# Kernel optimization log

Measured on AMD Instinct MI355X. Metric: run time of the kernel, lower is better.

The kernel has to match this reference:

```python
import jax, jax.numpy as jnp
import numpy as np

B, T, D, K = 64, 512, 1024, 50


def setup_inputs() -> dict:
    key = jax.random.key(0)
    ks = jax.random.split(key, 6)
    inputs = jax.random.normal(ks[0], (B, T, D), dtype=jnp.float32)
    mask = jnp.ones((B, T), dtype=jnp.int32)
    labels = jax.random.randint(ks[1], (B, T), 0, K)
    W = jax.random.normal(ks[2], (D, K), dtype=jnp.float32) / jnp.sqrt(jnp.float32(D))
    b = jnp.zeros((K,), dtype=jnp.float32)
    transitions = jax.random.normal(ks[3], (K, K), dtype=jnp.float32) * 0.1
    start_transitions = jax.random.normal(ks[4], (K,), dtype=jnp.float32) * 0.1
    end_transitions = jax.random.normal(ks[5], (K,), dtype=jnp.float32) * 0.1
    return dict(inputs=inputs, mask=mask, labels=labels, W=W, b=b,
                transitions=transitions, start_transitions=start_transitions,
                end_transitions=end_transitions)


def _log_partition(emissions, mask_f, trans, start, end):
    # emissions [B,T,K]; forward algorithm with logsumexp recurrence (lax.scan)
    alpha0 = start[None, :] + emissions[:, 0]  # [B,K]
    def step(alpha, xs):
        emit, m = xs  # [B,K], [B]
        inner = alpha[:, :, None] + trans[None, :, :] + emit[:, None, :]  # [B,K,K]
        new = jax.nn.logsumexp(inner, axis=1)
        alpha = jnp.where(m[:, None] > 0, new, alpha)  # carry state through padding
        return alpha, None
    emits = jnp.swapaxes(emissions[:, 1:], 0, 1)  # [T-1,B,K]
    ms = jnp.swapaxes(mask_f[:, 1:], 0, 1)
    alpha, _ = jax.lax.scan(step, alpha0, (emits, ms))
    return jax.nn.logsumexp(alpha + end[None, :], axis=1)  # [B]


def _gold_score(emissions, labels, mask_f, trans, start, end):
    emit_sc = jnp.take_along_axis(emissions, labels[..., None], axis=2)[..., 0]  # [B,T]
    emit_sum = jnp.sum(emit_sc * mask_f, axis=1)
    trans_sc = trans[labels[:, :-1], labels[:, 1:]]  # [B,T-1]
    trans_sum = jnp.sum(trans_sc * mask_f[:, 1:], axis=1)
    last_idx = jnp.sum(mask_f, axis=1).astype(jnp.int32) - 1
    last_tags = jnp.take_along_axis(labels, last_idx[:, None], axis=1)[:, 0]
    return start[labels[:, 0]] + emit_sum + trans_sum + end[last_tags]


def _viterbi(emissions, mask_f, trans, start, end):
    Bv, Tv, Kv = emissions.shape
    alpha0 = start[None, :] + emissions[:, 0]
    ident = jnp.broadcast_to(jnp.arange(Kv, dtype=jnp.int32)[None, :], (Bv, Kv))
    def step(alpha, xs):
        emit, m = xs
        inner = alpha[:, :, None] + trans[None, :, :]  # [B,K_prev,K_cur]
        bp = jnp.argmax(inner, axis=1).astype(jnp.int32)  # [B,K]
        new = jnp.max(inner, axis=1) + emit
        cond = m[:, None] > 0
        alpha = jnp.where(cond, new, alpha)
        bp = jnp.where(cond, bp, ident)  # padded step: tag carries through
        return alpha, bp
    emits = jnp.swapaxes(emissions[:, 1:], 0, 1)
    ms = jnp.swapaxes(mask_f[:, 1:], 0, 1)
    alpha, bps = jax.lax.scan(step, alpha0, (emits, ms))  # bps [T-1,B,K]
    last = jnp.argmax(alpha + end[None, :], axis=1).astype(jnp.int32)  # [B]
    def back(tag, bp):
        prev = jnp.take_along_axis(bp, tag[:, None], axis=1)[:, 0]
        return prev, tag
    first_tag, tags_rest = jax.lax.scan(back, last, bps, reverse=True)  # tags_rest[t]=tag at pos t+1
    tags = jnp.concatenate([first_tag[None, :], tags_rest], axis=0)  # [T,B]
    return jnp.swapaxes(tags, 0, 1)  # [B,T]


def reference(inputs, mask, labels, W, b, transitions, start_transitions, end_transitions):
    emissions = inputs @ W + b  # tag_projection: [B,T,K]
    mask_f = mask.astype(emissions.dtype)
    scores = emissions * mask_f[..., None]  # module masks logits before CRF
    tags = _viterbi(scores, mask_f, transitions, start_transitions, end_transitions)
    tags = tags * mask.astype(tags.dtype)
    ll = _gold_score(scores, labels, mask_f, transitions, start_transitions, end_transitions) \
         - _log_partition(scores, mask_f, transitions, start_transitions, end_transitions)
    loss = -jnp.sum(ll)  # reduction='sum' negative log-likelihood
    return scores, tags, loss
```

## Files before the change

kernel.cpp:

```cpp
#include <hip/hip_runtime.h>

#define B_ 64
#define T_ 512
#define D_ 1024
#define K_ 50

#define BM 256
#define BK 16

__global__ __launch_bounds__(256) void gemm_kernel(const float* __restrict__ A,
                                                   const float* __restrict__ W,
                                                   float* __restrict__ P0,
                                                   float* __restrict__ P1) {
  __shared__ float As[BM][20];
  __shared__ float Wt[56][20];

  const int tid = threadIdx.x;
  const int rowBase = blockIdx.x * BM;
  const int kh = blockIdx.y;
  const int kBase = kh * 512;
  float* __restrict__ P = kh ? P1 : P0;

  const int rg = tid & 31;
  const int cg = tid >> 5;

  float acc[8][7];
#pragma unroll
  for (int i = 0; i < 8; i++)
#pragma unroll
    for (int j = 0; j < 7; j++) acc[i][j] = 0.f;

  const int q = tid & 3;
  const int rr = tid >> 2;

  for (int ch = 0; ch < 512 / BK; ++ch) {
    const int kb = kBase + ch * BK;
#pragma unroll
    for (int s = 0; s < 4; s++) {
      const int r = rr + 64 * s;
      const float4 v = *(const float4*)&A[(size_t)(rowBase + r) * 1024 + kb + q * 4];
      *(float4*)&As[r][q * 4] = v;
    }
#pragma unroll
    for (int s = 0; s < 4; s++) {
      const int l = tid + 256 * s;
      if (l < 800) {
        const int kk = l / 50;
        const int c = l - kk * 50;
        Wt[c][kk] = W[(size_t)(kb + kk) * 50 + c];
      }
    }
    __syncthreads();
#pragma unroll
    for (int k4 = 0; k4 < BK; k4 += 4) {
      float4 a[8];
#pragma unroll
      for (int i = 0; i < 8; i++) a[i] = *(const float4*)&As[rg + 32 * i][k4];
#pragma unroll
      for (int j = 0; j < 7; j++) {
        const float4 w = *(const float4*)&Wt[cg * 7 + j][k4];
#pragma unroll
        for (int i = 0; i < 8; i++) {
          acc[i][j] += a[i].x * w.x + a[i].y * w.y + a[i].z * w.z + a[i].w * w.w;
        }
      }
    }
    __syncthreads();
  }
#pragma unroll
  for (int i = 0; i < 8; i++) {
    const int row = rowBase + rg + 32 * i;
#pragma unroll
    for (int j = 0; j < 7; j++) {
      const int c = cg * 7 + j;
      if (c < 50) P[(size_t)row * 50 + c] = acc[i][j];
    }
  }
}

__global__ __launch_bounds__(256) void combine_kernel(const float* __restrict__ P0,
                                                      const float* __restrict__ P1,
                                                      const float* __restrict__ bias,
                                                      const int* __restrict__ mask,
                                                      float* __restrict__ scores,
                                                      float* __restrict__ lossSlot) {
  const int idx = blockIdx.x * 256 + threadIdx.x;
  const int m = idx / 50;
  const int c = idx - m * 50;
  float v = P0[idx] + P1[idx] + bias[c];
  v *= (float)mask[m];
  scores[idx] = v;
  if (idx == 0) *lossSlot = 0.f;
}

__global__ __launch_bounds__(256) void crf_kernel(const float* __restrict__ scores,
                                                  const int* __restrict__ mask,
                                                  const int* __restrict__ labels,
                                                  const float* __restrict__ trans,
                                                  const float* __restrict__ startT,
                                                  const float* __restrict__ endT,
                                                  float* __restrict__ tagsOut,
                                                  float* __restrict__ lossSlot) {
  __shared__ float e_lds[64];
  __shared__ float ps_lds[2][4][64];
  __shared__ float av_lds[64];
  __shared__ float pv_lds[2][4][64];
  __shared__ int pj_lds[2][4][64];
  __shared__ unsigned char bp_s[511 * 52];
  __shared__ unsigned char g_s[32 * 52];
  __shared__ unsigned char chin_s[32];
  __shared__ float redp_s[4];
  __shared__ int redm_s[4];

  const int b = blockIdx.x;
  const int tid = threadIdx.x;
  const int wave = tid >> 6;
  const int lane = tid & 63;
  const int k = lane;
  const int kc = (k < 50) ? k : 49;

  const int j0s[4] = {0, 12, 24, 36};
  const int jns[4] = {12, 12, 12, 14};
  const int j0 = j0s[wave];
  const int jn = jns[wave];

  if (tid < 64) { e_lds[tid] = 0.f; av_lds[tid] = 0.f; }
  __syncthreads();

  const size_t sb = (size_t)b * T_ * 50;

  if (blockIdx.y == 0) {
    float eT[14];
#pragma unroll
    for (int jj = 0; jj < 14; jj++) {
      const int j = j0 + jj;
      eT[jj] = (jj < jn) ? __expf(trans[j * 50 + kc]) : 0.f;
    }
    float af = (k < 50) ? (startT[k] + scores[sb + k]) : -1e30f;
    float M = __int_as_float(__builtin_amdgcn_readfirstlane(__float_as_int(af)));
    float emit_next = scores[sb + 50 + kc];
    int mnext = mask[b * T_ + 1];
    int buf = 0;
    for (int t = 1; t < T_; ++t) {
      const float emit = emit_next;
      const int mt = mnext;
      if (t < T_ - 1) {
        emit_next = scores[sb + (size_t)(t + 1) * 50 + kc];
        mnext = mask[b * T_ + t + 1];
      }
      const float e = __expf(af - M);
      if (lane >= j0 && lane < j0 + jn) e_lds[lane] = e;
      float ev[16];
#pragma unroll
      for (int u = 0; u < 4; u++) *(float4*)&ev[4 * u] = *(const float4*)&e_lds[j0 + 4 * u];
      float ps = 0.f;
#pragma unroll
      for (int jj = 0; jj < 14; jj++) ps += ev[jj] * eT[jj];
      ps_lds[buf][wave][lane] = ps;
      __syncthreads();
      const float S = (ps_lds[buf][0][lane] + ps_lds[buf][1][lane]) +
                      (ps_lds[buf][2][lane] + ps_lds[buf][3][lane]);
      const float afn = M + __logf(S) + emit;
      af = (mt > 0) ? afn : af;
      M = __int_as_float(__builtin_amdgcn_readfirstlane(__float_as_int(af)));
      buf ^= 1;
    }
    const float x = (k < 50) ? (af + endT[k]) : -3e38f;
    float mx = x;
#pragma unroll
    for (int off = 32; off >= 1; off >>= 1) mx = fmaxf(mx, __shfl_xor(mx, off));
    float sm = (k < 50) ? __expf(x - mx) : 0.f;
#pragma unroll
    for (int off = 32; off >= 1; off >>= 1) sm += __shfl_xor(sm, off);
    const float logZ = mx + __logf(sm);
    float part = 0.f;
    int mcnt = 0;
#pragma unroll
    for (int s2 = 0; s2 < 2; s2++) {
      const int t = tid + 256 * s2;
      const int lt = labels[b * T_ + t];
      const int mt = mask[b * T_ + t];
      mcnt += mt;
      part += (mt > 0) ? scores[sb + (size_t)t * 50 + lt] : 0.f;
      if (t < T_ - 1) {
        const int ln = labels[b * T_ + t + 1];
        const int mn = mask[b * T_ + t + 1];
        part += (mn > 0) ? trans[lt * 50 + ln] : 0.f;
      }
    }
#pragma unroll
    for (int off = 32; off >= 1; off >>= 1) {
      part += __shfl_xor(part, off);
      mcnt += __shfl_xor(mcnt, off);
    }
    if (lane == 0) { redp_s[wave] = part; redm_s[wave] = mcnt; }
    __syncthreads();
    if (tid == 0) {
      float gold = redp_s[0] + redp_s[1] + redp_s[2] + redp_s[3];
      const int tot = redm_s[0] + redm_s[1] + redm_s[2] + redm_s[3];
      const int l0 = labels[b * T_];
      const int llast = labels[b * T_ + (tot - 1)];
      gold += startT[l0] + endT[llast];
      atomicAdd(lossSlot, -(gold - logZ));
    }
  } else {
    float Tv[14];
#pragma unroll
    for (int jj = 0; jj < 14; jj++) {
      const int j = j0 + jj;
      Tv[jj] = (jj < jn) ? trans[j * 50 + kc] : -1e30f;
    }
    float av = (k < 50) ? (startT[k] + scores[sb + k]) : -1e30f;
    float emit_next = scores[sb + 50 + kc];
    int mnext = mask[b * T_ + 1];
    int buf = 0;
    for (int t = 1; t < T_; ++t) {
      const float emit = emit_next;
      const int mt = mnext;
      if (t < T_ - 1) {
        emit_next = scores[sb + (size_t)(t + 1) * 50 + kc];
        mnext = mask[b * T_ + t + 1];
      }
      if (lane >= j0 && lane < j0 + jn) av_lds[lane] = av;
      float avv[16];
#pragma unroll
      for (int u = 0; u < 4; u++) *(float4*)&avv[4 * u] = *(const float4*)&av_lds[j0 + 4 * u];
      float best = -3e38f;
      int bj = 0;
#pragma unroll
      for (int jj = 0; jj < 14; jj++) {
        const float u = avv[jj] + Tv[jj];
        if (u > best) { best = u; bj = jj; }
      }
      pv_lds[buf][wave][lane] = best;
      pj_lds[buf][wave][lane] = j0 + bj;
      __syncthreads();
      float bv = pv_lds[buf][0][lane];
      int bi = pj_lds[buf][0][lane];
#pragma unroll
      for (int w = 1; w < 4; w++) {
        const float v2 = pv_lds[buf][w][lane];
        const int i2 = pj_lds[buf][w][lane];
        if (v2 > bv) { bv = v2; bi = i2; }
      }
      const bool upd = mt > 0;
      if (wave == 0 && k < 50) bp_s[(t - 1) * 52 + k] = (unsigned char)(upd ? bi : k);
      av = upd ? (bv + emit) : av;
      buf ^= 1;
    }
    float x = (k < 50) ? (av + endT[k]) : -3e38f;
    int xi = (k < 50) ? k : 63;
#pragma unroll
    for (int off = 32; off >= 1; off >>= 1) {
      const float ov = __shfl_xor(x, off);
      const int oi = __shfl_xor(xi, off);
      if (ov > x || (ov == x && oi < xi)) { x = ov; xi = oi; }
    }
    const int last = xi;
    __syncthreads();
    for (int p = 0; p < 7; p++) {
      const int idx = tid + 256 * p;
      if (idx < 1600) {
        const int c = idx / 50;
        const int s2 = idx - c * 50;
        int x2 = s2;
        const int lo = 16 * c;
        const int hi = min(16 * c + 15, 510);
        for (int i = hi; i >= lo; --i) x2 = bp_s[i * 52 + x2];
        g_s[c * 52 + s2] = (unsigned char)x2;
      }
    }
    __syncthreads();
    if (tid == 0) {
      int cur = last;
      chin_s[31] = (unsigned char)cur;
      for (int c = 31; c >= 1; --c) {
        cur = g_s[c * 52 + cur];
        chin_s[c - 1] = (unsigned char)cur;
      }
      const int m511 = mask[b * T_ + 511];
      tagsOut[(size_t)b * T_ + 511] = (float)((m511 > 0) ? last : 0);
    }
    __syncthreads();
    if (tid < 32) {
      const int c = tid;
      int x3 = chin_s[c];
      const int lo = 16 * c;
      const int hi = min(16 * c + 15, 510);
      for (int i = hi; i >= lo; --i) {
        x3 = bp_s[i * 52 + x3];
        const int mi = mask[b * T_ + i];
        tagsOut[(size_t)b * T_ + i] = (float)((mi > 0) ? x3 : 0);
      }
    }
  }
}

extern "C" void kernel_launch(void* const* d_in, const int* in_sizes, int n_in,
                              void* d_out, int out_size, void* d_ws, size_t ws_size,
                              hipStream_t stream) {
  const float* inputs = (const float*)d_in[0];
  const int* mask = (const int*)d_in[1];
  const int* labels = (const int*)d_in[2];
  const float* W = (const float*)d_in[3];
  const float* bias = (const float*)d_in[4];
  const float* trans = (const float*)d_in[5];
  const float* startT = (const float*)d_in[6];
  const float* endT = (const float*)d_in[7];

  float* out = (float*)d_out;
  float* scores = out;
  float* tagsOut = out + (size_t)B_ * T_ * K_;
  float* lossSlot = out + (size_t)B_ * T_ * K_ + B_ * T_;
  float* P1 = (float*)d_ws;

  dim3 g1(128, 2);
  gemm_kernel<<<g1, 256, 0, stream>>>(inputs, W, scores, P1);

  combine_kernel<<<(B_ * T_ * K_) / 256, 256, 0, stream>>>(scores, P1, bias, mask,
                                                           scores, lossSlot);

  dim3 g3(B_, 2);
  crf_kernel<<<g3, 256, 0, stream>>>(scores, mask, labels, trans, startT, endT,
                                     tagsOut, lossSlot);
}
```

Measured before the change: 586.1 us.

## Increase split-K parallelism in GEMM with swizzled LDS and column-major partials

Lets the split-K factor in the emission GEMM grow up to 8, picked from the workspace size, so more blocks are launched. It also reshapes the per-thread tile to 4x13, swizzles the shared-memory layout of A and W to avoid bank conflicts, and uses explicit fmaf chains. Partial results are now stored column-major in the workspace and reduced by the combine kernel. The cost is more partial-sum traffic in the combine kernel and possible extra register pressure under the occupancy hint of 4 blocks per SM.

```diff
diff --git a/kernel.cpp b/kernel.cpp
--- a/kernel.cpp
+++ b/kernel.cpp
@@ -4,92 +4,106 @@
 #define T_ 512
 #define D_ 1024
 #define K_ 50
-
-#define BM 256
-#define BK 16
-
-__global__ __launch_bounds__(256) void gemm_kernel(const float* __restrict__ A,
-                                                   const float* __restrict__ W,
-                                                   float* __restrict__ P0,
-                                                   float* __restrict__ P1) {
-  __shared__ float As[BM][20];
-  __shared__ float Wt[56][20];
+#define MROWS (B_ * T_)
+
+__global__ __launch_bounds__(256, 4) void gemm_kernel(const float* __restrict__ A,
+                                                      const float* __restrict__ W,
+                                                      float* __restrict__ P,
+                                                      int chunkK) {
+  __shared__ float As[256][20];
+  __shared__ float Wt[52][16];
 
   const int tid = threadIdx.x;
-  const int rowBase = blockIdx.x * BM;
-  const int kh = blockIdx.y;
-  const int kBase = kh * 512;
-  float* __restrict__ P = kh ? P1 : P0;
-
-  const int rg = tid & 31;
-  const int cg = tid >> 5;
-
-  float acc[8][7];
-#pragma unroll
-  for (int i = 0; i < 8; i++)
-#pragma unroll
-    for (int j = 0; j < 7; j++) acc[i][j] = 0.f;
+  const int rowBase = blockIdx.x * 256;
+  const int kBase = blockIdx.y * chunkK;
+  float* __restrict__ Pp = P + (size_t)blockIdx.y * K_ * MROWS;
+
+  const int rg = tid & 63;
+  const int cg = tid >> 6;
+  const int c0 = cg * 13;
+  const int swr = (rg >> 3) & 3;
+
+  float acc[4][13];
+#pragma unroll
+  for (int i = 0; i < 4; i++)
+#pragma unroll
+    for (int j = 0; j < 13; j++) acc[i][j] = 0.f;
 
   const int q = tid & 3;
   const int rr = tid >> 2;
 
-  for (int ch = 0; ch < 512 / BK; ++ch) {
-    const int kb = kBase + ch * BK;
+  const int iters = chunkK >> 4;
+  for (int ch = 0; ch < iters; ++ch) {
+    const int kb = kBase + (ch << 4);
 #pragma unroll
     for (int s = 0; s < 4; s++) {
       const int r = rr + 64 * s;
       const float4 v = *(const float4*)&A[(size_t)(rowBase + r) * 1024 + kb + q * 4];
-      *(float4*)&As[r][q * 4] = v;
+      const int p = (q + ((r >> 3) & 3)) & 3;
+      *(float4*)&As[r][p * 4] = v;
     }
 #pragma unroll
     for (int s = 0; s < 4; s++) {
       const int l = tid + 256 * s;
-      if (l < 800) {
-        const int kk = l / 50;
-        const int c = l - kk * 50;
-        Wt[c][kk] = W[(size_t)(kb + kk) * 50 + c];
-      }
-    }
-    __syncthreads();
-#pragma unroll
-    for (int k4 = 0; k4 < BK; k4 += 4) {
-      float4 a[8];
-#pragma unroll
-      for (int i = 0; i < 8; i++) a[i] = *(const float4*)&As[rg + 32 * i][k4];
-#pragma unroll
-      for (int j = 0; j < 7; j++) {
-        const float4 w = *(const float4*)&Wt[cg * 7 + j][k4];
-#pragma unroll
-        for (int i = 0; i < 8; i++) {
-          acc[i][j] += a[i].x * w.x + a[i].y * w.y + a[i].z * w.z + a[i].w * w.w;
+      if (l < 832) {
+        const int kk = l / 52;
+        const int c = l - kk * 52;
+        const float val = (c < 50) ? W[(size_t)(kb + kk) * 50 + c] : 0.f;
+        const int pq = ((kk >> 2) + (c >> 2)) & 3;
+        Wt[c][pq * 4 + (kk & 3)] = val;
+      }
+    }
+    __syncthreads();
+#pragma unroll
+    for (int k4 = 0; k4 < 4; k4++) {
+      float4 a[4];
+#pragma unroll
+      for (int i = 0; i < 4; i++)
+        a[i] = *(const float4*)&As[rg + 64 * i][((k4 + swr) & 3) * 4];
+#pragma unroll
+      for (int j = 0; j < 13; j++) {
+        const int c = c0 + j;
+        const float4 w = *(const float4*)&Wt[c][((k4 + (c >> 2)) & 3) * 4];
+#pragma unroll
+        for (int i = 0; i < 4; i++) {
+          float t = acc[i][j];
+          t = fmaf(a[i].x, w.x, t);
+          t = fmaf(a[i].y, w.y, t);
+          t = fmaf(a[i].z, w.z, t);
+          t = fmaf(a[i].w, w.w, t);
+          acc[i][j] = t;
         }
       }
     }
     __syncthreads();
   }
 #pragma unroll
-  for (int i = 0; i < 8; i++) {
-    const int row = rowBase + rg + 32 * i;
-#pragma unroll
-    for (int j = 0; j < 7; j++) {
-      const int c = cg * 7 + j;
-      if (c < 50) P[(size_t)row * 50 + c] = acc[i][j];
+  for (int j = 0; j < 13; j++) {
+    const int c = c0 + j;
+    if (c < 50) {
+#pragma unroll
+      for (int i = 0; i < 4; i++) {
+        Pp[(size_t)c * MROWS + rowBase + rg + 64 * i] = acc[i][j];
+      }
     }
   }
 }
 
-__global__ __launch_bounds__(256) void combine_kernel(const float* __restrict__ P0,
-                                                      const float* __restrict__ P1,
+__global__ __launch_bounds__(256) void combine_kernel(const float* __restrict__ P,
+                                                      int SK,
                                                       const float* __restrict__ bias,
                                                       const int* __restrict__ mask,
                                                       float* __restrict__ scores,
                                                       float* __restrict__ lossSlot) {
   const int idx = blockIdx.x * 256 + threadIdx.x;
-  const int m = idx / 50;
-  const int c = idx - m * 50;
-  float v = P0[idx] + P1[idx] + bias[c];
-  v *= (float)mask[m];
-  scores[idx] = v;
+  const int c = idx >> 15;
+  const int row = idx & 32767;
+  float s = 0.f;
+  for (int sk = 0; sk < SK; sk++)
+    s += P[(size_t)sk * K_ * MROWS + (size_t)c * MROWS + row];
+  s += bias[c];
+  s *= (float)mask[row];
+  scores[(size_t)row * 50 + c] = s;
   if (idx == 0) *lossSlot = 0.f;
 }
 
@@ -312,13 +326,21 @@
   float* scores = out;
   float* tagsOut = out + (size_t)B_ * T_ * K_;
   float* lossSlot = out + (size_t)B_ * T_ * K_ + B_ * T_;
-  float* P1 = (float*)d_ws;
-
-  dim3 g1(128, 2);
-  gemm_kernel<<<g1, 256, 0, stream>>>(inputs, W, scores, P1);
-
-  combine_kernel<<<(B_ * T_ * K_) / 256, 256, 0, stream>>>(scores, P1, bias, mask,
-                                                           scores, lossSlot);
+  float* P = (float*)d_ws;
+
+  const size_t per = (size_t)K_ * MROWS * sizeof(float);
+  int SK;
+  if (ws_size >= 8 * per) SK = 8;
+  else if (ws_size >= 4 * per) SK = 4;
+  else if (ws_size >= 2 * per) SK = 2;
+  else SK = 1;
+  const int chunkK = D_ / SK;
+
+  dim3 g1(MROWS / 256, SK);
+  gemm_kernel<<<g1, 256, 0, stream>>>(inputs, W, P, chunkK);
+
+  combine_kernel<<<(K_ * MROWS) / 256, 256, 0, stream>>>(P, SK, bias, mask,
+                                                         scores, lossSlot);
 
   dim3 g3(B_, 2);
   crf_kernel<<<g3, 256, 0, stream>>>(scores, mask, labels, trans, startT, endT,
```

Result: slower. 1.934 ms (+230.0%).
